# Performance work log

Measured on AMD Instinct MI355X. Metric: run time of the kernel, lower is better.

Reference implementation:

```python
import jax, jax.numpy as jnp
import numpy as np

NUM_HEADS = 16
ROPE_THETA = 10000.0


def _rope_cos_sin(seq_len, head_dim, dtype):
    # Llama rotary embedding: inv_freq over even dims, emb = cat(freqs, freqs)
    inv_freq = 1.0 / (ROPE_THETA ** (jnp.arange(0, head_dim, 2, dtype=jnp.float32) / head_dim))
    t = jnp.arange(seq_len, dtype=jnp.float32)
    freqs = jnp.outer(t, inv_freq)              # [S, hd/2]
    emb = jnp.concatenate([freqs, freqs], -1)   # [S, hd]
    return jnp.cos(emb).astype(dtype), jnp.sin(emb).astype(dtype)


def _rotate_half(x):
    h = x.shape[-1] // 2
    return jnp.concatenate([-x[..., h:], x[..., :h]], axis=-1)


def setup_inputs() -> dict:
    key = jax.random.key(0)
    ks = jax.random.split(key, 5)
    B, S, D = 1, 2048, 2048
    scale = 0.02
    return {
        "hidden_states": jax.random.normal(ks[0], (B, S, D), jnp.float32),
        "Wq": jax.random.normal(ks[1], (D, D), jnp.float32) * scale,
        "Wk": jax.random.normal(ks[2], (D, D), jnp.float32) * scale,
        "Wv": jax.random.normal(ks[3], (D, D), jnp.float32) * scale,
        "Wo": jax.random.normal(ks[4], (D, D), jnp.float32) * scale,
    }


def reference(hidden_states, Wq, Wk, Wv, Wo):
    B, S, D = hidden_states.shape
    H = NUM_HEADS
    hd = D // H
    sm_scale = 1.0 / np.sqrt(hd)

    # QKV projections (nn.Linear without bias: x @ W.T), kept in [B,S,H,hd]
    q = (hidden_states @ Wq.T).reshape(B, S, H, hd)
    k = (hidden_states @ Wk.T).reshape(B, S, H, hd)
    v = (hidden_states @ Wv.T).reshape(B, S, H, hd)

    # RoPE (offset=0, no kv cache)
    cos, sin = _rope_cos_sin(S, hd, hidden_states.dtype)
    cos = cos[None, :, None, :]  # [1,S,1,hd]
    sin = sin[None, :, None, :]
    q = q * cos + _rotate_half(q) * sin
    k = k * cos + _rotate_half(k) * sin

    # Causal self-attention (exact math of FlashSelfAttention(causal=True))
    scores = jnp.einsum("bshd,bthd->bhst", q, k) * sm_scale  # [B,H,S,S]
    causal = jnp.tril(jnp.ones((S, S), dtype=bool))
    scores = jnp.where(causal[None, None], scores, jnp.finfo(scores.dtype).min)
    probs = jax.nn.softmax(scores, axis=-1)
    attn = jnp.einsum("bhst,bthd->bshd", probs, v)           # [B,S,H,hd]

    # Output projection
    attn = attn.reshape(B, S, H * hd)
    return attn @ Wo.T
```

## Files before the change

### kernel.cpp

```cpp
#include <hip/hip_runtime.h>
#include <hip/hip_bf16.h>
#include <math.h>

#define S_LEN 2048
#define DMODEL 2048
#define NHEADS 16
#define HDIM 128

typedef __bf16 bf16x8 __attribute__((ext_vector_type(8)));
typedef float f32x4 __attribute__((ext_vector_type(4)));

__device__ __forceinline__ unsigned short f2b(float f) {
  union { float f; unsigned u; } c; c.f = f;
  unsigned r = (c.u + 0x7fffu + ((c.u >> 16) & 1u)) >> 16;
  return (unsigned short)r;
}
__device__ __forceinline__ float b2f(unsigned short b) {
  union { unsigned u; float f; } c; c.u = ((unsigned)b) << 16;
  return c.f;
}

__device__ __forceinline__ void gload_lds16(const unsigned short* g, unsigned short* l) {
  __builtin_amdgcn_global_load_lds(
      (__attribute__((address_space(1))) void*)(void*)g,
      (__attribute__((address_space(3))) void*)(void*)l, 16, 0, 0);
}

__global__ void cvt5_f32_bf16_k(const float* __restrict__ s0,
                                const float* __restrict__ s1,
                                const float* __restrict__ s2,
                                const float* __restrict__ s3,
                                const float* __restrict__ s4,
                                unsigned short* __restrict__ d0,
                                unsigned short* __restrict__ d1,
                                unsigned short* __restrict__ d2,
                                unsigned short* __restrict__ d3,
                                unsigned short* __restrict__ d4) {
  int gi = blockIdx.x * blockDim.x + threadIdx.x;
  int seg = gi >> 20;
  int i = (gi & 0xFFFFF) * 4;
  const float* src = (seg == 0) ? s0 : (seg == 1) ? s1 : (seg == 2) ? s2
                     : (seg == 3) ? s3 : s4;
  unsigned short* dst = (seg == 0) ? d0 : (seg == 1) ? d1 : (seg == 2) ? d2
                        : (seg == 3) ? d3 : d4;
  float4 v = *reinterpret_cast<const float4*>(src + i);
  ushort4 o;
  o.x = f2b(v.x); o.y = f2b(v.y); o.z = f2b(v.z); o.w = f2b(v.w);
  *reinterpret_cast<ushort4*>(dst + i) = o;
}

__global__ void rope_table_k(float* __restrict__ cs, float* __restrict__ sn) {
  int idx = blockIdx.x * blockDim.x + threadIdx.x;
  int s = idx >> 6, i = idx & 63;
  float inv = powf(10000.0f, -(float)(2 * i) / 128.0f);
  float a = (float)s * inv;
  cs[idx] = cosf(a);
  sn[idx] = sinf(a);
}

__global__ void rope_apply_k(unsigned short* __restrict__ q,
                             unsigned short* __restrict__ k,
                             const float* __restrict__ cs,
                             const float* __restrict__ sn) {
  const float SC = 0.08838834764831845f * 1.4426950408889634f;
  int idx = blockIdx.x * blockDim.x + threadIdx.x;
  int i = idx & 63;
  int h = (idx >> 6) & (NHEADS - 1);
  int s = idx >> 10;
  size_t base = (size_t)s * DMODEL + h * HDIM;
  float c = cs[s * 64 + i], sv = sn[s * 64 + i];
  float qc = c * SC, qs = sv * SC;
  float q1 = b2f(q[base + i]), q2 = b2f(q[base + i + 64]);
  q[base + i]      = f2b(q1 * qc - q2 * qs);
  q[base + i + 64] = f2b(q2 * qc + q1 * qs);
  float k1 = b2f(k[base + i]), k2 = b2f(k[base + i + 64]);
  k[base + i]      = f2b(k1 * c - k2 * sv);
  k[base + i + 64] = f2b(k2 * c + k1 * sv);
}

__global__ __launch_bounds__(256) void transpose_bf16_k(
    const unsigned short* __restrict__ in, unsigned short* __restrict__ out) {
  __shared__ unsigned short tile[64][72];
  int bx = blockIdx.x, by = blockIdx.y;
  int t = threadIdx.x;
#pragma unroll
  for (int i = 0; i < 2; ++i) {
    int ch = i * 256 + t;
    int r = ch >> 3, c8 = ch & 7;
    bf16x8 v = *reinterpret_cast<const bf16x8*>(
        in + (size_t)(by * 64 + r) * DMODEL + bx * 64 + c8 * 8);
    *reinterpret_cast<bf16x8*>(&tile[r][c8 * 8]) = v;
  }
  __syncthreads();
#pragma unroll
  for (int i = 0; i < 2; ++i) {
    int ch = i * 256 + t;
    int c = ch >> 3, r8 = ch & 7;
    union { bf16x8 v; unsigned short u[8]; } w;
#pragma unroll
    for (int j = 0; j < 8; ++j) w.u[j] = tile[r8 * 8 + j][c];
    *reinterpret_cast<bf16x8*>(
        out + (size_t)(bx * 64 + c) * S_LEN + by * 64 + r8 * 8) = w.v;
  }
}


#define MIDBAR_SEQ()                                      \
  do {                                                    \
    asm volatile("" ::: "memory");                        \
    __builtin_amdgcn_s_barrier();                         \
    asm volatile("s_waitcnt lgkmcnt(0)" ::: "memory");    \
    __builtin_amdgcn_sched_barrier(0);                    \
    __builtin_amdgcn_s_setprio(1);                        \
  } while (0)

#define ENDBAR_SEQ()                                      \
  do {                                                    \
    __builtin_amdgcn_s_setprio(0);                        \
    asm volatile("" ::: "memory");                        \
    __builtin_amdgcn_s_barrier();                         \
    asm volatile("" ::: "memory");                        \
  } while (0)

#define READA(QM)                                                              \
  do {                                                                         \
    _Pragma("unroll") for (int j = 0; j < MQ; ++j)                             \
    _Pragma("unroll") for (int kk = 0; kk < 2; ++kk) {                         \
      int row = wm * (BM / 2) + ((QM) * MQ + j) * 16 + li;                     \
      int c = (kk * 4 + g) ^ (li & 7);                                         \
      af[j][kk] = *reinterpret_cast<const bf16x8*>(&As[cur][row * 64 + c * 8]);\
    }                                                                          \
  } while (0)

#define READB(BF, QN)                                                          \
  do {                                                                         \
    _Pragma("unroll") for (int jn = 0; jn < 2; ++jn)                           \
    _Pragma("unroll") for (int kk = 0; kk < 2; ++kk) {                         \
      int row = wn * 64 + ((QN) * 2 + jn) * 16 + li;                           \
      int c = (kk * 4 + g) ^ (li & 7);                                         \
      BF[jn][kk] = *reinterpret_cast<const bf16x8*>(&Bs[cur][row * 64 + c * 8]);\
    }                                                                          \
  } while (0)

#define QUAD(QM, QN, BF)                                                       \
  do {                                                                         \
    _Pragma("unroll") for (int j = 0; j < MQ; ++j)                             \
    _Pragma("unroll") for (int jn = 0; jn < 2; ++jn)                           \
    _Pragma("unroll") for (int kk = 0; kk < 2; ++kk)                           \
      acc[(QM) * MQ + j][(QN) * 2 + jn] =                                      \
          __builtin_amdgcn_mfma_f32_16x16x32_bf16(                             \
              af[j][kk], BF[jn][kk], acc[(QM) * MQ + j][(QN) * 2 + jn], 0, 0, 0);\
  } while (0)

template <int BM, bool OUT_F32>
__global__ __launch_bounds__(512, 2) void gemm_8ph_k(
    const unsigned short* __restrict__ A, const unsigned short* __restrict__ B0p,
    const unsigned short* __restrict__ B1p, const unsigned short* __restrict__ B2p,
    void* __restrict__ C0, void* __restrict__ C1, void* __restrict__ C2,
    int M, int N, int K) {
  constexpr int MQ = BM / 64;
  constexpr int MR = BM / 32;

  __shared__ unsigned short As[2][BM * 64];
  __shared__ unsigned short Bs[2][256 * 64];

  const unsigned short* Bp = (blockIdx.z == 0) ? B0p : (blockIdx.z == 1) ? B1p : B2p;
  void* Cout = (blockIdx.z == 0) ? C0 : (blockIdx.z == 1) ? C1 : C2;

  int nwg = gridDim.x, bid = blockIdx.x;
  int wg = (bid & 7) * (nwg >> 3) + (bid >> 3);
  int ntn = N >> 8;
  int tm = wg / ntn, tn = wg % ntn;
  int m0 = tm * BM, n0 = tn << 8;

  const int tid = threadIdx.x;
  const int wave = tid >> 6, lane = tid & 63;
  const int g = lane >> 4, li = lane & 15;
  const int wm = wave >> 2, wn = wave & 3;

  auto stageB = [&](int buf, int tt, int qn) {
#pragma unroll
    for (int i = 0; i < 2; ++i) {
      int j = i * 512 + tid;
      int piece = j >> 8, rowin = (j >> 3) & 31, c = j & 7;
      int row = piece * 64 + qn * 32 + rowin;
      gload_lds16(Bp + (size_t)(n0 + row) * K + tt * 64 + ((c ^ (row & 7)) * 8),
                  &Bs[buf][row * 64 + c * 8]);
    }
  };
  auto stageA = [&](int buf, int tt, int qm) {
#pragma unroll
    for (int i = 0; i < BM / 128; ++i) {
      int j = i * 512 + tid;
      int piece = j / (2 * BM);
      int rowin = (j >> 3) & (BM / 4 - 1);
      int c = j & 7;
      int row = piece * (BM / 2) + qm * (BM / 4) + rowin;
      gload_lds16(A + (size_t)(m0 + row) * K + tt * 64 + ((c ^ (row & 7)) * 8),
                  &As[buf][row * 64 + c * 8]);
    }
  };

  f32x4 acc[MR][4];
#pragma unroll
  for (int i = 0; i < MR; ++i)
#pragma unroll
    for (int j = 0; j < 4; ++j) acc[i][j] = (f32x4){0.f, 0.f, 0.f, 0.f};

  const int nK = K >> 6;

  stageB(0, 0, 0); stageA(0, 0, 0); stageB(0, 0, 1); stageA(0, 0, 1);
  stageB(1, 1, 0); stageA(1, 1, 0); stageB(1, 1, 1); stageA(1, 1, 1);
  if constexpr (BM == 256) asm volatile("s_waitcnt vmcnt(8)" ::: "memory");
  else                     asm volatile("s_waitcnt vmcnt(6)" ::: "memory");
  asm volatile("" ::: "memory");
  __builtin_amdgcn_s_barrier();
  asm volatile("" ::: "memory");

  for (int t = 0; t < nK; ++t) {
    int cur = t & 1;
    bool pf = (t + 2 < nK);
    bf16x8 af[MQ][2], bf0[2][2], bf1[2][2];
    READA(0);
    READB(bf0, 0);
    MIDBAR_SEQ();
    QUAD(0, 0, bf0);
    ENDBAR_SEQ();
    READB(bf1, 1);
    if (pf) { stageB(cur, t + 2, 0); stageA(cur, t + 2, 0); }
    MIDBAR_SEQ();
    QUAD(0, 1, bf1);
    ENDBAR_SEQ();
    READA(1);
    if (pf) stageB(cur, t + 2, 1);
    MIDBAR_SEQ();
    QUAD(1, 1, bf1);
    ENDBAR_SEQ();
    if (pf) {
      stageA(cur, t + 2, 1);
      if constexpr (BM == 256) asm volatile("s_waitcnt vmcnt(8)" ::: "memory");
      else                     asm volatile("s_waitcnt vmcnt(6)" ::: "memory");
    } else {
      asm volatile("s_waitcnt vmcnt(0)" ::: "memory");
    }
    MIDBAR_SEQ();
    QUAD(1, 0, bf0);
    ENDBAR_SEQ();
  }

#pragma unroll
  for (int m = 0; m < MR; ++m) {
#pragma unroll
    for (int n = 0; n < 4; ++n) {
      int row = m0 + wm * (BM / 2) + m * 16 + g * 4;
      int col = n0 + wn * 64 + n * 16 + li;
#pragma unroll
      for (int r = 0; r < 4; ++r) {
        if (OUT_F32)
          reinterpret_cast<float*>(Cout)[(size_t)(row + r) * N + col] = acc[m][n][r];
        else
          reinterpret_cast<unsigned short*>(Cout)[(size_t)(row + r) * N + col] =
              f2b(acc[m][n][r]);
      }
    }
  }
}

#undef MIDBAR_SEQ
#undef ENDBAR_SEQ
#undef READA
#undef READB
#undef QUAD

__global__ __launch_bounds__(256) void flash_attn_k(
    const unsigned short* __restrict__ q, const unsigned short* __restrict__ k,
    const unsigned short* __restrict__ vt, unsigned short* __restrict__ o) {
  __shared__ unsigned short Ks[2][64 * 128];
  __shared__ unsigned short Vs[2][128 * 64];
  __shared__ unsigned short Ps[4 * 16 * 72];

  int L = blockIdx.x;
  int xcd = L & 7, j = L >> 3;
  int h = 2 * xcd + (j & 1);
  int qt = (j < 32) ? (31 - (j >> 1)) : ((j - 32) >> 1);

  int t = threadIdx.x, wave = t >> 6, lane = t & 63;
  int g = lane >> 4, li = lane & 15;
  int q0 = qt * 64;

  const unsigned short* vth = vt + (size_t)h * HDIM * S_LEN;

  auto stage = [&](int buf, int kt) {
    int kv0 = kt * 64;
#pragma unroll
    for (int i = 0; i < 4; ++i) {
      int ch = i * 256 + t;
      int row = ch >> 4, c = ch & 15;
      int cs_ = c ^ (row & 7);
      gload_lds16(k + (size_t)(kv0 + row) * DMODEL + h * HDIM + cs_ * 8,
                  &Ks[buf][ch * 8]);
    }
#pragma unroll
    for (int i = 0; i < 4; ++i) {
      int ch = i * 256 + t;
      int row = ch >> 3, c = ch & 7;
      int cs_ = c ^ (row & 7);
      gload_lds16(vth + (size_t)row * S_LEN + kv0 + cs_ * 8,
                  &Vs[buf][ch * 8]);
    }
  };

  int qrow = q0 + wave * 16 + li;
  bf16x8 qf[4];
#pragma unroll
  for (int kb = 0; kb < 4; ++kb)
    qf[kb] = *reinterpret_cast<const bf16x8*>(
        q + (size_t)qrow * DMODEL + h * HDIM + kb * 32 + g * 8);

  bf16x8 ones;
#pragma unroll
  for (int jj = 0; jj < 8; ++jj) ones[jj] = (__bf16)1.0f;

  f32x4 O[8];
#pragma unroll
  for (int db = 0; db < 8; ++db) O[db] = (f32x4){0.f, 0.f, 0.f, 0.f};
  f32x4 lA = (f32x4){0.f, 0.f, 0.f, 0.f};
  float m_r[4];
#pragma unroll
  for (int r = 0; r < 4; ++r) m_r[r] = -1e30f;

  auto tile_body = [&](int it, int cur, bool diag) {
    int kv0 = it * 64;
    f32x4 sf[4];
#pragma unroll
    for (int jb = 0; jb < 4; ++jb) sf[jb] = (f32x4){0.f, 0.f, 0.f, 0.f};
#pragma unroll
    for (int kb = 0; kb < 4; ++kb) {
#pragma unroll
      for (int jb = 0; jb < 4; ++jb) {
        int row = jb * 16 + li;
        int c = (kb * 4 + g) ^ (row & 7);
        bf16x8 kf = *reinterpret_cast<const bf16x8*>(&Ks[cur][row * 128 + c * 8]);
        sf[jb] = __builtin_amdgcn_mfma_f32_16x16x32_bf16(qf[kb], kf, sf[jb], 0, 0, 0);
      }
    }

    float pm[4] = {-1e30f, -1e30f, -1e30f, -1e30f};
    if (diag) {
#pragma unroll
      for (int jb = 0; jb < 4; ++jb) {
        int jcol = kv0 + jb * 16 + li;
#pragma unroll
        for (int r = 0; r < 4; ++r) {
          int irow = q0 + wave * 16 + g * 4 + r;
          if (jcol > irow) sf[jb][r] = -1e30f;
          pm[r] = fmaxf(pm[r], sf[jb][r]);
        }
      }
    } else {
#pragma unroll
      for (int jb = 0; jb < 4; ++jb)
#pragma unroll
        for (int r = 0; r < 4; ++r) pm[r] = fmaxf(pm[r], sf[jb][r]);
    }
#pragma unroll
    for (int r = 0; r < 4; ++r) {
      float x = pm[r];
      x = fmaxf(x, __shfl_xor(x, 1));
      x = fmaxf(x, __shfl_xor(x, 2));
      x = fmaxf(x, __shfl_xor(x, 4));
      x = fmaxf(x, __shfl_xor(x, 8));
      pm[r] = x;
    }
    float alpha[4];
#pragma unroll
    for (int r = 0; r < 4; ++r) {
      float nm = fmaxf(m_r[r], pm[r]);
      alpha[r] = exp2f(m_r[r] - nm);
      m_r[r] = nm;
    }
#pragma unroll
    for (int jb = 0; jb < 4; ++jb)
#pragma unroll
      for (int r = 0; r < 4; ++r)
        Ps[wave * 16 * 72 + (g * 4 + r) * 72 + jb * 16 + li] =
            f2b(exp2f(sf[jb][r] - m_r[r]));
#pragma unroll
    for (int db = 0; db < 8; ++db)
#pragma unroll
      for (int r = 0; r < 4; ++r) O[db][r] *= alpha[r];
#pragma unroll
    for (int r = 0; r < 4; ++r) lA[r] *= alpha[r];

#pragma unroll
    for (int ks = 0; ks < 2; ++ks) {
      bf16x8 pa = *reinterpret_cast<const bf16x8*>(
          Ps + wave * 16 * 72 + li * 72 + ks * 32 + g * 8);
      lA = __builtin_amdgcn_mfma_f32_16x16x32_bf16(pa, ones, lA, 0, 0, 0);
#pragma unroll
      for (int db = 0; db < 8; ++db) {
        int row = db * 16 + li;
        int c = (ks * 4 + g) ^ (row & 7);
        bf16x8 vbf = *reinterpret_cast<const bf16x8*>(&Vs[cur][row * 64 + c * 8]);
        O[db] = __builtin_amdgcn_mfma_f32_16x16x32_bf16(pa, vbf, O[db], 0, 0, 0);
      }
    }
  };

  stage(0, 0);

  for (int it = 0; it < qt; ++it) {
    int cur = it & 1;
    stage(cur ^ 1, it + 1);
    asm volatile("s_waitcnt vmcnt(8)" ::: "memory");
    __builtin_amdgcn_s_barrier();
    asm volatile("" ::: "memory");
    tile_body(it, cur, false);
    __builtin_amdgcn_s_barrier();
    asm volatile("" ::: "memory");
  }
  {
    int cur = qt & 1;
    asm volatile("s_waitcnt vmcnt(0)" ::: "memory");
    __builtin_amdgcn_s_barrier();
    asm volatile("" ::: "memory");
    tile_body(qt, cur, true);
  }

#pragma unroll
  for (int db = 0; db < 8; ++db) {
#pragma unroll
    for (int r = 0; r < 4; ++r) {
      int row = q0 + wave * 16 + g * 4 + r;
      o[(size_t)row * DMODEL + h * HDIM + db * 16 + li] = f2b(O[db][r] / lA[r]);
    }
  }
}

extern "C" void kernel_launch(void* const* d_in, const int* in_sizes, int n_in,
                              void* d_out, int out_size, void* d_ws, size_t ws_size,
                              hipStream_t stream) {
  const float* hs = (const float*)d_in[0];
  const float* Wq = (const float*)d_in[1];
  const float* Wk = (const float*)d_in[2];
  const float* Wv = (const float*)d_in[3];
  const float* Wo = (const float*)d_in[4];

  char* ws = (char*)d_ws;
  const size_t MB = 1024 * 1024;
  unsigned short* hs_b = (unsigned short*)(ws + 0 * MB);
  unsigned short* Wq_b = (unsigned short*)(ws + 8 * MB);
  unsigned short* Wk_b = (unsigned short*)(ws + 16 * MB);
  unsigned short* Wv_b = (unsigned short*)(ws + 24 * MB);
  unsigned short* Wo_b = (unsigned short*)(ws + 32 * MB);
  unsigned short* qb = (unsigned short*)(ws + 40 * MB);
  unsigned short* kb = (unsigned short*)(ws + 48 * MB);
  unsigned short* vb = (unsigned short*)(ws + 56 * MB);
  unsigned short* ab = (unsigned short*)(ws + 64 * MB);
  float* cs = (float*)(ws + 72 * MB);
  float* sn = (float*)(ws + 72 * MB + 512 * 1024);
  unsigned short* vtb = hs_b;

  cvt5_f32_bf16_k<<<(5 * 1024 * 1024) / 256, 256, 0, stream>>>(
      hs, Wq, Wk, Wv, Wo, hs_b, Wq_b, Wk_b, Wv_b, Wo_b);

  rope_table_k<<<(S_LEN * 64) / 256, 256, 0, stream>>>(cs, sn);

  gemm_8ph_k<256, false><<<dim3(64, 1, 3), 512, 0, stream>>>(
      hs_b, Wq_b, Wk_b, Wv_b, qb, kb, vb, 2048, 2048, 2048);

  transpose_bf16_k<<<dim3(32, 32), 256, 0, stream>>>(vb, vtb);

  rope_apply_k<<<(S_LEN * NHEADS * 64) / 256, 256, 0, stream>>>(qb, kb, cs, sn);

  flash_attn_k<<<dim3(512), 256, 0, stream>>>(qb, kb, vtb, ab);

  gemm_8ph_k<128, true><<<dim3(128, 1, 1), 512, 0, stream>>>(
      ab, Wo_b, Wo_b, Wo_b, d_out, d_out, d_out, 2048, 2048, 2048);
}
```

Before: 218.8 us.

## Split KV range across two wave pairs and pair causal query tiles per block

The flash attention kernel now launches half as many blocks. Each block processes two query tiles, p and 31-p, so every block gets an equal share of the causal work. Inside a block, two pairs of waves each handle alternating KV tiles, and each wave now covers 32 query rows instead of 16. The two partial softmax states are merged through shared memory at the end. This balances load and doubles K/V reuse per LDS read, at the cost of twice the LDS footprint, more registers, extra barriers, and a merge step.

```diff
diff --git a/kernel.cpp b/kernel.cpp
--- a/kernel.cpp
+++ b/kernel.cpp
@@ -275,165 +275,251 @@
 __global__ __launch_bounds__(256) void flash_attn_k(
     const unsigned short* __restrict__ q, const unsigned short* __restrict__ k,
     const unsigned short* __restrict__ vt, unsigned short* __restrict__ o) {
-  __shared__ unsigned short Ks[2][64 * 128];
-  __shared__ unsigned short Vs[2][128 * 64];
-  __shared__ unsigned short Ps[4 * 16 * 72];
+  __shared__ unsigned short Ks[2][2][64 * 128];
+  __shared__ unsigned short Vs[2][2][128 * 64];
+  __shared__ unsigned short Ps[4][32 * 72];
 
   int L = blockIdx.x;
   int xcd = L & 7, j = L >> 3;
   int h = 2 * xcd + (j & 1);
-  int qt = (j < 32) ? (31 - (j >> 1)) : ((j - 32) >> 1);
-
-  int t = threadIdx.x, wave = t >> 6, lane = t & 63;
-  int g = lane >> 4, li = lane & 15;
-  int q0 = qt * 64;
+  int p = j >> 1;
+
+  int t = threadIdx.x, wave = t >> 6, lane64 = t & 63;
+  int g = lane64 >> 4, li = lane64 & 15;
+  int ln = wave >> 1, w2 = wave & 1;
+  int tl = t & 127;
 
   const unsigned short* vth = vt + (size_t)h * HDIM * S_LEN;
 
-  auto stage = [&](int buf, int kt) {
+  auto stageKV = [&](int buf, int kt) {
     int kv0 = kt * 64;
 #pragma unroll
-    for (int i = 0; i < 4; ++i) {
-      int ch = i * 256 + t;
+    for (int i = 0; i < 8; ++i) {
+      int ch = i * 128 + tl;
       int row = ch >> 4, c = ch & 15;
       int cs_ = c ^ (row & 7);
       gload_lds16(k + (size_t)(kv0 + row) * DMODEL + h * HDIM + cs_ * 8,
-                  &Ks[buf][ch * 8]);
-    }
-#pragma unroll
-    for (int i = 0; i < 4; ++i) {
-      int ch = i * 256 + t;
+                  &Ks[ln][buf][ch * 8]);
+    }
+#pragma unroll
+    for (int i = 0; i < 8; ++i) {
+      int ch = i * 128 + tl;
       int row = ch >> 3, c = ch & 7;
       int cs_ = c ^ (row & 7);
       gload_lds16(vth + (size_t)row * S_LEN + kv0 + cs_ * 8,
-                  &Vs[buf][ch * 8]);
+                  &Vs[ln][buf][ch * 8]);
     }
   };
 
-  int qrow = q0 + wave * 16 + li;
-  bf16x8 qf[4];
-#pragma unroll
-  for (int kb = 0; kb < 4; ++kb)
-    qf[kb] = *reinterpret_cast<const bf16x8*>(
-        q + (size_t)qrow * DMODEL + h * HDIM + kb * 32 + g * 8);
-
   bf16x8 ones;
 #pragma unroll
   for (int jj = 0; jj < 8; ++jj) ones[jj] = (__bf16)1.0f;
 
-  f32x4 O[8];
-#pragma unroll
-  for (int db = 0; db < 8; ++db) O[db] = (f32x4){0.f, 0.f, 0.f, 0.f};
-  f32x4 lA = (f32x4){0.f, 0.f, 0.f, 0.f};
-  float m_r[4];
-#pragma unroll
-  for (int r = 0; r < 4; ++r) m_r[r] = -1e30f;
-
-  auto tile_body = [&](int it, int cur, bool diag) {
-    int kv0 = it * 64;
-    f32x4 sf[4];
-#pragma unroll
-    for (int jb = 0; jb < 4; ++jb) sf[jb] = (f32x4){0.f, 0.f, 0.f, 0.f};
-#pragma unroll
-    for (int kb = 0; kb < 4; ++kb) {
-#pragma unroll
-      for (int jb = 0; jb < 4; ++jb) {
-        int row = jb * 16 + li;
-        int c = (kb * 4 + g) ^ (row & 7);
-        bf16x8 kf = *reinterpret_cast<const bf16x8*>(&Ks[cur][row * 128 + c * 8]);
-        sf[jb] = __builtin_amdgcn_mfma_f32_16x16x32_bf16(qf[kb], kf, sf[jb], 0, 0, 0);
+  float* OM = (float*)&Ks[0][0][0];
+  float* ML = (float*)&Vs[0][0][0];
+
+  for (int seg = 0; seg < 2; ++seg) {
+    int qt = seg ? (31 - p) : p;
+    int q0 = qt * 64;
+    int nj = (qt + 2) >> 1;
+
+    bf16x8 qf[2][4];
+#pragma unroll
+    for (int mi = 0; mi < 2; ++mi)
+#pragma unroll
+      for (int kb = 0; kb < 4; ++kb)
+        qf[mi][kb] = *reinterpret_cast<const bf16x8*>(
+            q + (size_t)(q0 + w2 * 32 + mi * 16 + li) * DMODEL + h * HDIM +
+            kb * 32 + g * 8);
+
+    f32x4 O[2][8];
+#pragma unroll
+    for (int mi = 0; mi < 2; ++mi)
+#pragma unroll
+      for (int db = 0; db < 8; ++db) O[mi][db] = (f32x4){0.f, 0.f, 0.f, 0.f};
+    f32x4 lac[2] = {(f32x4){0.f, 0.f, 0.f, 0.f}, (f32x4){0.f, 0.f, 0.f, 0.f}};
+    float m_r[2][4];
+#pragma unroll
+    for (int mi = 0; mi < 2; ++mi)
+#pragma unroll
+      for (int r = 0; r < 4; ++r) m_r[mi][r] = -1e30f;
+
+    if (ln <= qt) stageKV(0, ln);
+
+    for (int jj = 0; jj < nj; ++jj) {
+      int cur = jj & 1;
+      int myt = 2 * jj + ln;
+      bool havec = (myt <= qt);
+      bool haven = (jj + 1 < nj) && (myt + 2 <= qt);
+      if (haven) {
+        stageKV(cur ^ 1, myt + 2);
+        asm volatile("s_waitcnt vmcnt(16)" ::: "memory");
+      } else {
+        asm volatile("s_waitcnt vmcnt(0)" ::: "memory");
       }
-    }
-
-    float pm[4] = {-1e30f, -1e30f, -1e30f, -1e30f};
-    if (diag) {
-#pragma unroll
-      for (int jb = 0; jb < 4; ++jb) {
-        int jcol = kv0 + jb * 16 + li;
-#pragma unroll
-        for (int r = 0; r < 4; ++r) {
-          int irow = q0 + wave * 16 + g * 4 + r;
-          if (jcol > irow) sf[jb][r] = -1e30f;
-          pm[r] = fmaxf(pm[r], sf[jb][r]);
+      __builtin_amdgcn_s_barrier();
+      asm volatile("" ::: "memory");
+
+      if (havec) {
+        int kv0 = myt * 64;
+        bool diag = (myt == qt);
+        f32x4 sf[2][4];
+#pragma unroll
+        for (int mi = 0; mi < 2; ++mi)
+#pragma unroll
+          for (int jb = 0; jb < 4; ++jb) sf[mi][jb] = (f32x4){0.f, 0.f, 0.f, 0.f};
+#pragma unroll
+        for (int kb = 0; kb < 4; ++kb) {
+#pragma unroll
+          for (int jb = 0; jb < 4; ++jb) {
+            int row = jb * 16 + li;
+            int c = (kb * 4 + g) ^ (row & 7);
+            bf16x8 kf = *reinterpret_cast<const bf16x8*>(
+                &Ks[ln][cur][row * 128 + c * 8]);
+            sf[0][jb] = __builtin_amdgcn_mfma_f32_16x16x32_bf16(
+                qf[0][kb], kf, sf[0][jb], 0, 0, 0);
+            sf[1][jb] = __builtin_amdgcn_mfma_f32_16x16x32_bf16(
+                qf[1][kb], kf, sf[1][jb], 0, 0, 0);
+          }
+        }
+
+        float pm[2][4];
+#pragma unroll
+        for (int mi = 0; mi < 2; ++mi)
+#pragma unroll
+          for (int r = 0; r < 4; ++r) pm[mi][r] = -1e30f;
+        if (diag) {
+#pragma unroll
+          for (int mi = 0; mi < 2; ++mi)
+#pragma unroll
+            for (int jb = 0; jb < 4; ++jb) {
+              int jcol = kv0 + jb * 16 + li;
+#pragma unroll
+              for (int r = 0; r < 4; ++r) {
+                int irow = q0 + w2 * 32 + mi * 16 + g * 4 + r;
+                if (jcol > irow) sf[mi][jb][r] = -1e30f;
+                pm[mi][r] = fmaxf(pm[mi][r], sf[mi][jb][r]);
+              }
+            }
+        } else {
+#pragma unroll
+          for (int mi = 0; mi < 2; ++mi)
+#pragma unroll
+            for (int jb = 0; jb < 4; ++jb)
+#pragma unroll
+              for (int r = 0; r < 4; ++r)
+                pm[mi][r] = fmaxf(pm[mi][r], sf[mi][jb][r]);
+        }
+#pragma unroll
+        for (int mi = 0; mi < 2; ++mi)
+#pragma unroll
+          for (int r = 0; r < 4; ++r) {
+            float x = pm[mi][r];
+            x = fmaxf(x, __shfl_xor(x, 1));
+            x = fmaxf(x, __shfl_xor(x, 2));
+            x = fmaxf(x, __shfl_xor(x, 4));
+            x = fmaxf(x, __shfl_xor(x, 8));
+            pm[mi][r] = x;
+          }
+        float alpha[2][4];
+#pragma unroll
+        for (int mi = 0; mi < 2; ++mi)
+#pragma unroll
+          for (int r = 0; r < 4; ++r) {
+            float nm = fmaxf(m_r[mi][r], pm[mi][r]);
+            alpha[mi][r] = exp2f(m_r[mi][r] - nm);
+            m_r[mi][r] = nm;
+          }
+#pragma unroll
+        for (int mi = 0; mi < 2; ++mi)
+#pragma unroll
+          for (int jb = 0; jb < 4; ++jb)
+#pragma unroll
+            for (int r = 0; r < 4; ++r)
+              Ps[wave][(mi * 16 + g * 4 + r) * 72 + jb * 16 + li] =
+                  f2b(exp2f(sf[mi][jb][r] - m_r[mi][r]));
+#pragma unroll
+        for (int mi = 0; mi < 2; ++mi) {
+#pragma unroll
+          for (int db = 0; db < 8; ++db)
+#pragma unroll
+            for (int r = 0; r < 4; ++r) O[mi][db][r] *= alpha[mi][r];
+#pragma unroll
+          for (int r = 0; r < 4; ++r) lac[mi][r] *= alpha[mi][r];
+        }
+
+#pragma unroll
+        for (int ks = 0; ks < 2; ++ks) {
+          bf16x8 pa0 = *reinterpret_cast<const bf16x8*>(
+              &Ps[wave][(li) * 72 + ks * 32 + g * 8]);
+          bf16x8 pa1 = *reinterpret_cast<const bf16x8*>(
+              &Ps[wave][(16 + li) * 72 + ks * 32 + g * 8]);
+          lac[0] = __builtin_amdgcn_mfma_f32_16x16x32_bf16(pa0, ones, lac[0], 0, 0, 0);
+          lac[1] = __builtin_amdgcn_mfma_f32_16x16x32_bf16(pa1, ones, lac[1], 0, 0, 0);
+#pragma unroll
+          for (int db = 0; db < 8; ++db) {
+            int row = db * 16 + li;
+            int c = (ks * 4 + g) ^ (row & 7);
+            bf16x8 vbf = *reinterpret_cast<const bf16x8*>(
+                &Vs[ln][cur][row * 64 + c * 8]);
+            O[0][db] = __builtin_amdgcn_mfma_f32_16x16x32_bf16(pa0, vbf, O[0][db], 0, 0, 0);
+            O[1][db] = __builtin_amdgcn_mfma_f32_16x16x32_bf16(pa1, vbf, O[1][db], 0, 0, 0);
+          }
         }
       }
-    } else {
-#pragma unroll
-      for (int jb = 0; jb < 4; ++jb)
-#pragma unroll
-        for (int r = 0; r < 4; ++r) pm[r] = fmaxf(pm[r], sf[jb][r]);
-    }
-#pragma unroll
-    for (int r = 0; r < 4; ++r) {
-      float x = pm[r];
-      x = fmaxf(x, __shfl_xor(x, 1));
-      x = fmaxf(x, __shfl_xor(x, 2));
-      x = fmaxf(x, __shfl_xor(x, 4));
-      x = fmaxf(x, __shfl_xor(x, 8));
-      pm[r] = x;
-    }
-    float alpha[4];
-#pragma unroll
-    for (int r = 0; r < 4; ++r) {
-      float nm = fmaxf(m_r[r], pm[r]);
-      alpha[r] = exp2f(m_r[r] - nm);
-      m_r[r] = nm;
-    }
-#pragma unroll
-    for (int jb = 0; jb < 4; ++jb)
-#pragma unroll
-      for (int r = 0; r < 4; ++r)
-        Ps[wave * 16 * 72 + (g * 4 + r) * 72 + jb * 16 + li] =
-            f2b(exp2f(sf[jb][r] - m_r[r]));
-#pragma unroll
-    for (int db = 0; db < 8; ++db)
-#pragma unroll
-      for (int r = 0; r < 4; ++r) O[db][r] *= alpha[r];
-#pragma unroll
-    for (int r = 0; r < 4; ++r) lA[r] *= alpha[r];
-
-#pragma unroll
-    for (int ks = 0; ks < 2; ++ks) {
-      bf16x8 pa = *reinterpret_cast<const bf16x8*>(
-          Ps + wave * 16 * 72 + li * 72 + ks * 32 + g * 8);
-      lA = __builtin_amdgcn_mfma_f32_16x16x32_bf16(pa, ones, lA, 0, 0, 0);
-#pragma unroll
-      for (int db = 0; db < 8; ++db) {
-        int row = db * 16 + li;
-        int c = (ks * 4 + g) ^ (row & 7);
-        bf16x8 vbf = *reinterpret_cast<const bf16x8*>(&Vs[cur][row * 64 + c * 8]);
-        O[db] = __builtin_amdgcn_mfma_f32_16x16x32_bf16(pa, vbf, O[db], 0, 0, 0);
+      __builtin_amdgcn_s_barrier();
+      asm volatile("" ::: "memory");
+    }
+
+    if (ln == 0) {
+#pragma unroll
+      for (int mi = 0; mi < 2; ++mi)
+#pragma unroll
+        for (int db = 0; db < 8; ++db)
+#pragma unroll
+          for (int r = 0; r < 4; ++r) {
+            int row = w2 * 32 + mi * 16 + g * 4 + r;
+            OM[row * 128 + db * 16 + li] = O[mi][db][r];
+          }
+      if (li == 0) {
+#pragma unroll
+        for (int mi = 0; mi < 2; ++mi)
+#pragma unroll
+          for (int r = 0; r < 4; ++r) {
+            int row = w2 * 32 + mi * 16 + g * 4 + r;
+            ML[row] = m_r[mi][r];
+            ML[64 + row] = lac[mi][r];
+          }
       }
     }
-  };
-
-  stage(0, 0);
-
-  for (int it = 0; it < qt; ++it) {
-    int cur = it & 1;
-    stage(cur ^ 1, it + 1);
-    asm volatile("s_waitcnt vmcnt(8)" ::: "memory");
     __builtin_amdgcn_s_barrier();
     asm volatile("" ::: "memory");
-    tile_body(it, cur, false);
+    if (ln == 1) {
+#pragma unroll
+      for (int mi = 0; mi < 2; ++mi) {
+        float eA[4], eB[4], inv[4];
+#pragma unroll
+        for (int r = 0; r < 4; ++r) {
+          int row = w2 * 32 + mi * 16 + g * 4 + r;
+          float mAv = ML[row], lAv = ML[64 + row];
+          float ms = fmaxf(mAv, m_r[mi][r]);
+          eA[r] = exp2f(mAv - ms);
+          eB[r] = exp2f(m_r[mi][r] - ms);
+          inv[r] = 1.0f / (lAv * eA[r] + lac[mi][r] * eB[r]);
+        }
+#pragma unroll
+        for (int db = 0; db < 8; ++db)
+#pragma unroll
+          for (int r = 0; r < 4; ++r) {
+            int row = w2 * 32 + mi * 16 + g * 4 + r;
+            float val = (OM[row * 128 + db * 16 + li] * eA[r] +
+                         O[mi][db][r] * eB[r]) * inv[r];
+            o[(size_t)(q0 + row) * DMODEL + h * HDIM + db * 16 + li] = f2b(val);
+          }
+      }
+    }
     __builtin_amdgcn_s_barrier();
     asm volatile("" ::: "memory");
-  }
-  {
-    int cur = qt & 1;
-    asm volatile("s_waitcnt vmcnt(0)" ::: "memory");
-    __builtin_amdgcn_s_barrier();
-    asm volatile("" ::: "memory");
-    tile_body(qt, cur, true);
-  }
-
-#pragma unroll
-  for (int db = 0; db < 8; ++db) {
-#pragma unroll
-    for (int r = 0; r < 4; ++r) {
-      int row = q0 + wave * 16 + g * 4 + r;
-      o[(size_t)row * DMODEL + h * HDIM + db * 16 + li] = f2b(O[db][r] / lA[r]);
-    }
   }
 }
 
@@ -473,7 +559,7 @@
 
   rope_apply_k<<<(S_LEN * NHEADS * 64) / 256, 256, 0, stream>>>(qb, kb, cs, sn);
 
-  flash_attn_k<<<dim3(512), 256, 0, stream>>>(qb, kb, vtb, ab);
+  flash_attn_k<<<dim3(256), 256, 0, stream>>>(qb, kb, vtb, ab);
 
   gemm_8ph_k<128, true><<<dim3(128, 1, 1), 512, 0, stream>>>(
       ab, Wo_b, Wo_b, Wo_b, d_out, d_out, d_out, 2048, 2048, 2048);
```

New measurement: 218.1 us. Within noise of the previous version (-0.3%).

## Rework flash attention with 32x32 MFMA, split-KV wave pairs, and register P

Applied to the files above, without the earlier changes.

The flash-attention kernel now uses 32x32x16 MFMAs with a transposed S^T/O^T formulation, so the probability tile stays in registers (packed with cvt_pk plus lane shuffles) instead of round-tripping through LDS. The four waves split into two KV-parity groups that each process alternate KV tiles. Two tiles are staged per iteration. Partial softmax states are merged through shared memory at the end, and the output is written with vectorized 16-byte stores. This targets LDS traffic and MFMA issue overhead, at the cost of larger LDS use (double-buffered pairs of tiles), more registers, and extra barriers in the merge.

```diff
diff --git a/kernel.cpp b/kernel.cpp
--- a/kernel.cpp
+++ b/kernel.cpp
@@ -9,6 +9,7 @@
 
 typedef __bf16 bf16x8 __attribute__((ext_vector_type(8)));
 typedef float f32x4 __attribute__((ext_vector_type(4)));
+typedef float f32x16 __attribute__((ext_vector_type(16)));
 
 __device__ __forceinline__ unsigned short f2b(float f) {
   union { float f; unsigned u; } c; c.f = f;
@@ -275,164 +276,214 @@
 __global__ __launch_bounds__(256) void flash_attn_k(
     const unsigned short* __restrict__ q, const unsigned short* __restrict__ k,
     const unsigned short* __restrict__ vt, unsigned short* __restrict__ o) {
-  __shared__ unsigned short Ks[2][64 * 128];
-  __shared__ unsigned short Vs[2][128 * 64];
-  __shared__ unsigned short Ps[4 * 16 * 72];
+  __shared__ unsigned short Ks[2][2][64 * 128];
+  __shared__ unsigned short Vs[2][2][128 * 64];
 
   int L = blockIdx.x;
   int xcd = L & 7, j = L >> 3;
   int h = 2 * xcd + (j & 1);
   int qt = (j < 32) ? (31 - (j >> 1)) : ((j - 32) >> 1);
 
-  int t = threadIdx.x, wave = t >> 6, lane = t & 63;
-  int g = lane >> 4, li = lane & 15;
+  int t = threadIdx.x, wave = t >> 6, l = t & 63;
+  int l5 = l >> 5, l31 = l & 31;
+  int par = wave >> 1, qh = wave & 1;
   int q0 = qt * 64;
+  int q_abs = q0 + qh * 32 + l31;
 
   const unsigned short* vth = vt + (size_t)h * HDIM * S_LEN;
 
-  auto stage = [&](int buf, int kt) {
-    int kv0 = kt * 64;
-#pragma unroll
-    for (int i = 0; i < 4; ++i) {
-      int ch = i * 256 + t;
-      int row = ch >> 4, c = ch & 15;
-      int cs_ = c ^ (row & 7);
-      gload_lds16(k + (size_t)(kv0 + row) * DMODEL + h * HDIM + cs_ * 8,
-                  &Ks[buf][ch * 8]);
-    }
-#pragma unroll
-    for (int i = 0; i < 4; ++i) {
-      int ch = i * 256 + t;
-      int row = ch >> 3, c = ch & 7;
-      int cs_ = c ^ (row & 7);
-      gload_lds16(vth + (size_t)row * S_LEN + kv0 + cs_ * 8,
-                  &Vs[buf][ch * 8]);
+  auto stage = [&](int buf, int itv) {
+#pragma unroll
+    for (int p2 = 0; p2 < 2; ++p2) {
+      int kv0 = (2 * itv + p2) * 64;
+#pragma unroll
+      for (int i = 0; i < 4; ++i) {
+        int ch = i * 256 + t;
+        int row = ch >> 4, c = ch & 15;
+        gload_lds16(k + (size_t)(kv0 + row) * DMODEL + h * HDIM + ((c ^ (row & 7)) * 8),
+                    &Ks[p2][buf][ch * 8]);
+      }
+#pragma unroll
+      for (int i = 0; i < 4; ++i) {
+        int ch = i * 256 + t;
+        int row = ch >> 3, c = ch & 7;
+        gload_lds16(vth + (size_t)row * S_LEN + kv0 + ((c ^ (row & 7)) * 8),
+                    &Vs[p2][buf][ch * 8]);
+      }
     }
   };
 
-  int qrow = q0 + wave * 16 + li;
-  bf16x8 qf[4];
-#pragma unroll
-  for (int kb = 0; kb < 4; ++kb)
+  bf16x8 qf[8];
+#pragma unroll
+  for (int kb = 0; kb < 8; ++kb)
     qf[kb] = *reinterpret_cast<const bf16x8*>(
-        q + (size_t)qrow * DMODEL + h * HDIM + kb * 32 + g * 8);
-
-  bf16x8 ones;
-#pragma unroll
-  for (int jj = 0; jj < 8; ++jj) ones[jj] = (__bf16)1.0f;
-
-  f32x4 O[8];
-#pragma unroll
-  for (int db = 0; db < 8; ++db) O[db] = (f32x4){0.f, 0.f, 0.f, 0.f};
-  f32x4 lA = (f32x4){0.f, 0.f, 0.f, 0.f};
-  float m_r[4];
-#pragma unroll
-  for (int r = 0; r < 4; ++r) m_r[r] = -1e30f;
-
-  auto tile_body = [&](int it, int cur, bool diag) {
-    int kv0 = it * 64;
-    f32x4 sf[4];
-#pragma unroll
-    for (int jb = 0; jb < 4; ++jb) sf[jb] = (f32x4){0.f, 0.f, 0.f, 0.f};
-#pragma unroll
-    for (int kb = 0; kb < 4; ++kb) {
-#pragma unroll
-      for (int jb = 0; jb < 4; ++jb) {
-        int row = jb * 16 + li;
-        int c = (kb * 4 + g) ^ (row & 7);
-        bf16x8 kf = *reinterpret_cast<const bf16x8*>(&Ks[cur][row * 128 + c * 8]);
-        sf[jb] = __builtin_amdgcn_mfma_f32_16x16x32_bf16(qf[kb], kf, sf[jb], 0, 0, 0);
-      }
-    }
-
-    float pm[4] = {-1e30f, -1e30f, -1e30f, -1e30f};
-    if (diag) {
-#pragma unroll
-      for (int jb = 0; jb < 4; ++jb) {
-        int jcol = kv0 + jb * 16 + li;
-#pragma unroll
-        for (int r = 0; r < 4; ++r) {
-          int irow = q0 + wave * 16 + g * 4 + r;
-          if (jcol > irow) sf[jb][r] = -1e30f;
-          pm[r] = fmaxf(pm[r], sf[jb][r]);
-        }
-      }
+        q + (size_t)q_abs * DMODEL + h * HDIM + kb * 16 + l5 * 8);
+
+  f32x16 OT[4];
+#pragma unroll
+  for (int nf = 0; nf < 4; ++nf)
+#pragma unroll
+    for (int r = 0; r < 16; ++r) OT[nf][r] = 0.f;
+  float m_r = -1e30f, l_r = 0.f;
+
+  int nIter = (qt >> 1) + 1;
+  stage(0, 0);
+
+  for (int it = 0; it < nIter; ++it) {
+    int cur = it & 1;
+    if (it + 1 < nIter) {
+      stage(cur ^ 1, it + 1);
+      asm volatile("s_waitcnt vmcnt(16)" ::: "memory");
     } else {
-#pragma unroll
-      for (int jb = 0; jb < 4; ++jb)
-#pragma unroll
-        for (int r = 0; r < 4; ++r) pm[r] = fmaxf(pm[r], sf[jb][r]);
-    }
-#pragma unroll
-    for (int r = 0; r < 4; ++r) {
-      float x = pm[r];
-      x = fmaxf(x, __shfl_xor(x, 1));
-      x = fmaxf(x, __shfl_xor(x, 2));
-      x = fmaxf(x, __shfl_xor(x, 4));
-      x = fmaxf(x, __shfl_xor(x, 8));
-      pm[r] = x;
-    }
-    float alpha[4];
-#pragma unroll
-    for (int r = 0; r < 4; ++r) {
-      float nm = fmaxf(m_r[r], pm[r]);
-      alpha[r] = exp2f(m_r[r] - nm);
-      m_r[r] = nm;
-    }
-#pragma unroll
-    for (int jb = 0; jb < 4; ++jb)
-#pragma unroll
-      for (int r = 0; r < 4; ++r)
-        Ps[wave * 16 * 72 + (g * 4 + r) * 72 + jb * 16 + li] =
-            f2b(exp2f(sf[jb][r] - m_r[r]));
-#pragma unroll
-    for (int db = 0; db < 8; ++db)
-#pragma unroll
-      for (int r = 0; r < 4; ++r) O[db][r] *= alpha[r];
-#pragma unroll
-    for (int r = 0; r < 4; ++r) lA[r] *= alpha[r];
-
-#pragma unroll
-    for (int ks = 0; ks < 2; ++ks) {
-      bf16x8 pa = *reinterpret_cast<const bf16x8*>(
-          Ps + wave * 16 * 72 + li * 72 + ks * 32 + g * 8);
-      lA = __builtin_amdgcn_mfma_f32_16x16x32_bf16(pa, ones, lA, 0, 0, 0);
-#pragma unroll
-      for (int db = 0; db < 8; ++db) {
-        int row = db * 16 + li;
-        int c = (ks * 4 + g) ^ (row & 7);
-        bf16x8 vbf = *reinterpret_cast<const bf16x8*>(&Vs[cur][row * 64 + c * 8]);
-        O[db] = __builtin_amdgcn_mfma_f32_16x16x32_bf16(pa, vbf, O[db], 0, 0, 0);
-      }
-    }
-  };
-
-  stage(0, 0);
-
-  for (int it = 0; it < qt; ++it) {
-    int cur = it & 1;
-    stage(cur ^ 1, it + 1);
-    asm volatile("s_waitcnt vmcnt(8)" ::: "memory");
+      asm volatile("s_waitcnt vmcnt(0)" ::: "memory");
+    }
     __builtin_amdgcn_s_barrier();
     asm volatile("" ::: "memory");
-    tile_body(it, cur, false);
+
+    int myt = 2 * it + par;
+    if (myt <= qt) {
+      int kv0 = myt * 64;
+      f32x16 sf[2];
+#pragma unroll
+      for (int kvs = 0; kvs < 2; ++kvs)
+#pragma unroll
+        for (int r = 0; r < 16; ++r) sf[kvs][r] = 0.f;
+#pragma unroll
+      for (int kb = 0; kb < 8; ++kb) {
+#pragma unroll
+        for (int kvs = 0; kvs < 2; ++kvs) {
+          int row = kvs * 32 + l31;
+          int c = (2 * kb + l5) ^ (row & 7);
+          bf16x8 kf = *reinterpret_cast<const bf16x8*>(&Ks[par][cur][row * 128 + c * 8]);
+          sf[kvs] = __builtin_amdgcn_mfma_f32_32x32x16_bf16(kf, qf[kb], sf[kvs], 0, 0, 0);
+        }
+      }
+      if (myt == qt) {
+#pragma unroll
+        for (int kvs = 0; kvs < 2; ++kvs)
+#pragma unroll
+          for (int r = 0; r < 16; ++r) {
+            int kv_abs = kv0 + kvs * 32 + (r & 3) + 8 * (r >> 2) + 4 * l5;
+            if (kv_abs > q_abs) sf[kvs][r] = -1e30f;
+          }
+      }
+      float pm = -1e30f;
+#pragma unroll
+      for (int kvs = 0; kvs < 2; ++kvs)
+#pragma unroll
+        for (int r = 0; r < 16; ++r) pm = fmaxf(pm, sf[kvs][r]);
+      pm = fmaxf(pm, __shfl_xor(pm, 32));
+      float nm = fmaxf(m_r, pm);
+      float alpha = exp2f(m_r - nm);
+      m_r = nm;
+      float ls = 0.f;
+#pragma unroll
+      for (int kvs = 0; kvs < 2; ++kvs)
+#pragma unroll
+        for (int r = 0; r < 16; ++r) {
+          float pv = exp2f(sf[kvs][r] - nm);
+          sf[kvs][r] = pv;
+          ls += pv;
+        }
+      l_r = l_r * alpha + ls + __shfl_xor(ls, 32);
+#pragma unroll
+      for (int nf = 0; nf < 4; ++nf)
+#pragma unroll
+        for (int r = 0; r < 16; ++r) OT[nf][r] *= alpha;
+
+      bf16x8 pf[4];
+#pragma unroll
+      for (int ks = 0; ks < 4; ++ks) {
+        const int kvs = ks >> 1;
+        const int m0 = 8 * (ks & 1);
+        unsigned A0, A1, B0, B1;
+        asm("v_cvt_pk_bf16_f32 %0, %1, %2" : "=v"(A0) : "v"(sf[kvs][m0 + 0]), "v"(sf[kvs][m0 + 1]));
+        asm("v_cvt_pk_bf16_f32 %0, %1, %2" : "=v"(A1) : "v"(sf[kvs][m0 + 2]), "v"(sf[kvs][m0 + 3]));
+        asm("v_cvt_pk_bf16_f32 %0, %1, %2" : "=v"(B0) : "v"(sf[kvs][m0 + 4]), "v"(sf[kvs][m0 + 5]));
+        asm("v_cvt_pk_bf16_f32 %0, %1, %2" : "=v"(B1) : "v"(sf[kvs][m0 + 6]), "v"(sf[kvs][m0 + 7]));
+        unsigned rA0 = (unsigned)__shfl_xor((int)A0, 32);
+        unsigned rA1 = (unsigned)__shfl_xor((int)A1, 32);
+        unsigned rB0 = (unsigned)__shfl_xor((int)B0, 32);
+        unsigned rB1 = (unsigned)__shfl_xor((int)B1, 32);
+        union { unsigned u[4]; bf16x8 v; } pk;
+        pk.u[0] = l5 ? rB0 : A0;
+        pk.u[1] = l5 ? rB1 : A1;
+        pk.u[2] = l5 ? B0 : rA0;
+        pk.u[3] = l5 ? B1 : rA1;
+        pf[ks] = pk.v;
+      }
+
+#pragma unroll
+      for (int ks = 0; ks < 4; ++ks) {
+#pragma unroll
+        for (int nf = 0; nf < 4; ++nf) {
+          int row = nf * 32 + l31;
+          int c = (2 * ks + l5) ^ (row & 7);
+          bf16x8 vf = *reinterpret_cast<const bf16x8*>(&Vs[par][cur][row * 64 + c * 8]);
+          OT[nf] = __builtin_amdgcn_mfma_f32_32x32x16_bf16(vf, pf[ks], OT[nf], 0, 0, 0);
+        }
+      }
+    }
     __builtin_amdgcn_s_barrier();
     asm volatile("" ::: "memory");
   }
+
+  float* MS = (float*)&Ks[0][0][0];
+  float* ML = MS + 8192;
+  if (par == 1) {
+#pragma unroll
+    for (int nf = 0; nf < 4; ++nf)
+#pragma unroll
+      for (int r = 0; r < 16; ++r) {
+        int d = nf * 32 + (r & 3) + 8 * (r >> 2) + 4 * l5;
+        MS[qh * 4096 + d * 32 + l31] = OT[nf][r];
+      }
+    if (l < 32) { ML[qh * 64 + l31] = m_r; ML[qh * 64 + 32 + l31] = l_r; }
+  }
+  __builtin_amdgcn_s_barrier();
+  asm volatile("" ::: "memory");
+  if (par == 0) {
+    float mB = ML[qh * 64 + l31], lB = ML[qh * 64 + 32 + l31];
+    float ms = fmaxf(m_r, mB);
+    float eA = exp2f(m_r - ms), eB = exp2f(mB - ms);
+    float inv = 1.0f / (l_r * eA + lB * eB);
+#pragma unroll
+    for (int nf = 0; nf < 4; ++nf)
+#pragma unroll
+      for (int r = 0; r < 16; ++r) {
+        int d = nf * 32 + (r & 3) + 8 * (r >> 2) + 4 * l5;
+        OT[nf][r] = (OT[nf][r] * eA + MS[qh * 4096 + d * 32 + l31] * eB) * inv;
+      }
+  }
+  __builtin_amdgcn_s_barrier();
+  asm volatile("" ::: "memory");
+  if (par == 0) {
+#pragma unroll
+    for (int nf = 0; nf < 4; ++nf)
+#pragma unroll
+      for (int r = 0; r < 16; ++r) {
+        int d = nf * 32 + (r & 3) + 8 * (r >> 2) + 4 * l5;
+        MS[qh * 4096 + d * 32 + l31] = OT[nf][r];
+      }
+  }
+  __builtin_amdgcn_s_barrier();
+  asm volatile("" ::: "memory");
   {
-    int cur = qt & 1;
-    asm volatile("s_waitcnt vmcnt(0)" ::: "memory");
-    __builtin_amdgcn_s_barrier();
-    asm volatile("" ::: "memory");
-    tile_body(qt, cur, true);
-  }
-
-#pragma unroll
-  for (int db = 0; db < 8; ++db) {
-#pragma unroll
-    for (int r = 0; r < 4; ++r) {
-      int row = q0 + wave * 16 + g * 4 + r;
-      o[(size_t)row * DMODEL + h * HDIM + db * 16 + li] = f2b(O[db][r] / lA[r]);
+    int qq = t >> 2;
+    int dg = (t & 3) * 32;
+    const float* src = MS + (qq >> 5) * 4096 + (qq & 31);
+    unsigned pk[16];
+#pragma unroll
+    for (int i = 0; i < 16; ++i) {
+      unsigned lo = f2b(src[(dg + 2 * i) * 32]);
+      unsigned hi = f2b(src[(dg + 2 * i + 1) * 32]);
+      pk[i] = lo | (hi << 16);
+    }
+    unsigned short* op = o + (size_t)(q0 + qq) * DMODEL + h * HDIM + dg;
+#pragma unroll
+    for (int i = 0; i < 4; ++i) {
+      uint4 w = make_uint4(pk[4 * i], pk[4 * i + 1], pk[4 * i + 2], pk[4 * i + 3]);
+      *reinterpret_cast<uint4*>(op + i * 8) = w;
     }
   }
 }
```

Measured after the change: 215.3 us. No clear change (-1.6%).
